# Kernel tuning notes

Measured on AMD Instinct MI355X. Metric: run time of the kernel, lower is better.

Reference implementation:

```python
import jax, jax.numpy as jnp
import numpy as np

N_NODES = 50000
N_EDGES = 800000
IN_FEATURES = 256
HIDDEN = 128


def setup_inputs() -> dict:
    key = jax.random.key(0)
    k_x, k_r, k_c, k_v, k_w, k_b = jax.random.split(key, 6)
    x = jax.random.normal(k_x, (N_NODES, IN_FEATURES), dtype=jnp.float32)
    adj_row = jax.random.randint(k_r, (N_EDGES,), 0, N_NODES, dtype=jnp.int32)
    adj_col = jax.random.randint(k_c, (N_EDGES,), 0, N_NODES, dtype=jnp.int32)
    adj_val = jax.random.uniform(k_v, (N_EDGES,), dtype=jnp.float32)
    # Linear params: weight [hidden, in_features] (xavier-normal-ish), bias [hidden]
    std = float(np.sqrt(2.0 / (IN_FEATURES + HIDDEN)))
    W = jax.random.normal(k_w, (HIDDEN, IN_FEATURES), dtype=jnp.float32) * std
    b = jax.random.normal(k_b, (HIDDEN,), dtype=jnp.float32) * 0.01
    return {"x": x, "adj_row": adj_row, "adj_col": adj_col, "adj_val": adj_val, "W": W, "b": b}


def reference(x, adj_row, adj_col, adj_val, W, b):
    # support = Linear(x): [N, hidden]
    support = jnp.einsum('nf,hf->nh', x, W) + b
    # sparse adj @ support via edge-list gather + segment-sum scatter
    gathered = support[adj_col] * adj_val[:, None]          # [E, hidden]
    out = jax.ops.segment_sum(gathered, adj_row, num_segments=N_NODES)  # [N, hidden]
    return out
```

## Files before the change

kernel.cpp:

```cpp
#include <hip/hip_runtime.h>

#define N_NODES 50000
#define N_EDGES 800000
#define IN_F    256
#define HIDDEN  128

#define BUCKET_SZ 64
#define NB        782
#define NBINS     1024
#define EBLOCK    3328
#define EPT       13
#define EBLOCKS   241
#define LIN_ROWS  128
#define LBLOCKS   391
#define NTASKS    632
#define OFST_W    256
#define CAP       1300

#define SMEM_BYTES 35840

typedef __attribute__((ext_vector_type(8))) short bf16x8;
typedef __attribute__((ext_vector_type(4))) float f32x4;

__device__ inline unsigned short f2bf(float f) {
    unsigned u = __float_as_uint(f);
    u += 0x7FFF + ((u >> 16) & 1);
    return (unsigned short)(u >> 16);
}
__device__ inline bf16x8 cvt8(float4 a, float4 b) {
    bf16x8 r;
    r[0] = (short)f2bf(a.x); r[1] = (short)f2bf(a.y);
    r[2] = (short)f2bf(a.z); r[3] = (short)f2bf(a.w);
    r[4] = (short)f2bf(b.x); r[5] = (short)f2bf(b.y);
    r[6] = (short)f2bf(b.z); r[7] = (short)f2bf(b.w);
    return r;
}
__device__ inline float bfLo(unsigned u) { return __uint_as_float(u << 16); }
__device__ inline float bfHi(unsigned u) { return __uint_as_float(u & 0xFFFF0000u); }

__global__ __launch_bounds__(256) void fused_linear_partition_kernel(
    const float* __restrict__ x, const float* __restrict__ W,
    const float* __restrict__ bias, unsigned short* __restrict__ support,
    const int* __restrict__ adj_row, const int* __restrict__ adj_col,
    const float* __restrict__ adj_val,
    int2* __restrict__ part, int* __restrict__ ofsT)
{
    __shared__ __align__(16) char smem[SMEM_BYTES];
    const int tid = threadIdx.x;

    if (blockIdx.x < EBLOCKS) {
        int2* lbuf = (int2*)smem;
        int*  lofs = (int*)(smem + 26624);
        int*  lcur = (int*)(smem + 30720);
        int*  tsum = (int*)(smem + 34816);

        const int task = blockIdx.x;
        const int base = task * EBLOCK;
        const int n    = min(EBLOCK, N_EDGES - base);

        for (int i = tid; i < NBINS; i += 256) lofs[i] = 0;
        __syncthreads();

        unsigned pk[EPT]; float pv[EPT];
#pragma unroll
        for (int i = 0; i < EPT; ++i) {
            int li = tid + i * 256;
            bool ok = li < n;
            int ee = ok ? (base + li) : base;
            int r = adj_row[ee], c = adj_col[ee];
            float v = adj_val[ee];
            if (ok) {
                unsigned bk = (unsigned)r >> 6;
                pk[i] = (bk << 22) | (((unsigned)r & 63u) << 16) | (unsigned)c;
                pv[i] = v;
                atomicAdd(&lofs[bk], 1);
            } else pk[i] = 0xFFFFFFFFu;
        }
        __syncthreads();

        int s0 = lofs[tid * 4], s1 = lofs[tid * 4 + 1];
        int s2 = lofs[tid * 4 + 2], s3 = lofs[tid * 4 + 3];
        int mysum = s0 + s1 + s2 + s3;
        tsum[tid] = mysum;
        __syncthreads();
#pragma unroll
        for (int off = 1; off < 256; off <<= 1) {
            int t = (tid >= off) ? tsum[tid - off] : 0;
            __syncthreads();
            tsum[tid] += t;
            __syncthreads();
        }
        int ex = tsum[tid] - mysum;
        lofs[tid * 4]     = ex;
        lofs[tid * 4 + 1] = ex + s0;
        lofs[tid * 4 + 2] = ex + s0 + s1;
        lofs[tid * 4 + 3] = ex + s0 + s1 + s2;
        __syncthreads();

        for (int i = tid; i < NBINS; i += 256) lcur[i] = lofs[i];
        __syncthreads();

#pragma unroll
        for (int i = 0; i < EPT; ++i) {
            if (pk[i] != 0xFFFFFFFFu) {
                unsigned bk = pk[i] >> 22;
                int p = atomicAdd(&lcur[bk], 1);
                lbuf[p] = make_int2((int)(pk[i] & 0x3FFFFF), __float_as_int(pv[i]));
            }
        }
        __syncthreads();

        for (int j = tid; j < n; j += 256)
            part[(size_t)task * EBLOCK + j] = lbuf[j];
        for (int i = tid; i <= NB; i += 256)
            ofsT[(size_t)i * OFST_W + task] = lofs[i];
    } else {
        short* wfrag = (short*)smem;

        const int bid  = blockIdx.x - EBLOCKS;
        const int lane = tid & 63;
        const int wave = tid >> 6;
        const int quad = lane >> 4;
        const int l16  = lane & 15;

        int m0 = bid * LIN_ROWS + wave * 32 + l16;
        int m1 = m0 + 16;
        if (m0 >= N_NODES) m0 = N_NODES - 1;
        if (m1 >= N_NODES) m1 = N_NODES - 1;
        const float* xr0 = x + (size_t)m0 * IN_F;
        const float* xr1 = x + (size_t)m1 * IN_F;

        f32x4 acc[2][8];
#pragma unroll
        for (int g = 0; g < 2; ++g)
#pragma unroll
            for (int s = 0; s < 8; ++s) acc[g][s] = (f32x4){0.f, 0.f, 0.f, 0.f};

#pragma unroll
        for (int half = 0; half < 2; ++half) {
#pragma unroll
            for (int it = 0; it < 8; ++it) {
                const int f   = it * 256 + tid;
                const int ln  = f & 63;
                const int s   = (f >> 6) & 7;
                const int kc  = f >> 9;
                const int row = s * 16 + (ln & 15);
                const int k0  = (half * 4 + kc) * 32 + (ln >> 4) * 8;
                const float* wp = W + (size_t)row * IN_F + k0;
                float4 b0 = *(const float4*)wp;
                float4 b1 = *(const float4*)(wp + 4);
                *(bf16x8*)(&wfrag[(size_t)f * 8]) = cvt8(b0, b1);
            }
            __syncthreads();

#pragma unroll
            for (int kc = 0; kc < 4; ++kc) {
                const int k0 = (half * 4 + kc) * 32 + quad * 8;
                float4 a0 = *(const float4*)(xr0 + k0);
                float4 a1 = *(const float4*)(xr0 + k0 + 4);
                bf16x8 af0 = cvt8(a0, a1);
                float4 a2 = *(const float4*)(xr1 + k0);
                float4 a3 = *(const float4*)(xr1 + k0 + 4);
                bf16x8 af1 = cvt8(a2, a3);
                const short* bbase = &wfrag[((size_t)(kc * 8) * 64 + lane) * 8];
#pragma unroll
                for (int s = 0; s < 8; ++s) {
                    bf16x8 bf = *(const bf16x8*)(bbase + (size_t)s * 64 * 8);
                    acc[0][s] = __builtin_amdgcn_mfma_f32_16x16x32_bf16(af0, bf, acc[0][s], 0, 0, 0);
                    acc[1][s] = __builtin_amdgcn_mfma_f32_16x16x32_bf16(af1, bf, acc[1][s], 0, 0, 0);
                }
            }
            __syncthreads();
        }

#pragma unroll
        for (int g = 0; g < 2; ++g) {
            const int rowBase = bid * LIN_ROWS + wave * 32 + g * 16 + quad * 4;
#pragma unroll
            for (int reg = 0; reg < 4; ++reg) {
                const int r = rowBase + reg;
                if (r < N_NODES) {
#pragma unroll
                    for (int s = 0; s < 8; ++s) {
                        const int col = s * 16 + l16;
                        float v = acc[g][s][reg] + bias[col];
                        support[(size_t)r * HIDDEN + col] = f2bf(v);
                    }
                }
            }
        }
    }
}

__global__ __launch_bounds__(512) void bucket_gather_kernel(
    const int* __restrict__ ofsT, const int2* __restrict__ part,
    const unsigned int* __restrict__ support_u32, float* __restrict__ out)
{
    __shared__ int2 sbufA[CAP];
    __shared__ int2 sbufB[CAP];
    __shared__ int  wsum[8];
    __shared__ int  hist[BUCKET_SZ];
    __shared__ int  rp[BUCKET_SZ + 1];
    __shared__ int  cur[BUCKET_SZ];

    const int tid  = threadIdx.x;
    const int b    = blockIdx.x;
    const int wave = tid >> 6;
    const int lane = tid & 63;

    if (tid < BUCKET_SZ) hist[tid] = 0;

    int s0 = 0, slen = 0;
    if (tid < EBLOCKS) {
        s0   = ofsT[(size_t)b * OFST_W + tid];
        slen = ofsT[(size_t)(b + 1) * OFST_W + tid] - s0;
    }

    int iv = slen;
#pragma unroll
    for (int off = 1; off < 64; off <<= 1) {
        int t = __shfl_up(iv, off);
        if (lane >= off) iv += t;
    }
    if (lane == 63) wsum[wave] = iv;
    __syncthreads();
    int wpre = 0, total = 0;
#pragma unroll
    for (int w = 0; w < 8; ++w) {
        int sw = wsum[w];
        total += sw;
        if (w < wave) wpre += sw;
    }
    const int excl = wpre + iv - slen;
    const int n    = min(total, CAP);

    {
        const int2* seg = part + (size_t)tid * EBLOCK + s0;
        for (int k = 0; k < slen; ++k) {
            int p = excl + k;
            if (p < CAP) {
                int2 cv = seg[k];
                sbufA[p] = cv;
                atomicAdd(&hist[(cv.x >> 16) & 63], 1);
            }
        }
    }
    __syncthreads();

    if (tid < 64) {
        int a = hist[tid];
        int ia = a;
#pragma unroll
        for (int off = 1; off < 64; off <<= 1) {
            int t = __shfl_up(ia, off);
            if (tid >= off) ia += t;
        }
        rp[tid + 1] = ia;
        if (tid == 0) rp[0] = 0;
        cur[tid] = ia - a;
    }
    __syncthreads();

    for (int j = tid; j < n; j += 512) {
        int2 cv = sbufA[j];
        int p = atomicAdd(&cur[(cv.x >> 16) & 63], 1);
        sbufB[p] = cv;
    }
    __syncthreads();

    const int rowLo = wave * 8;
#pragma unroll 1
    for (int r = rowLo; r < rowLo + 8; ++r) {
        const int grow = b * BUCKET_SZ + r;
        if (grow >= N_NODES) break;
        const int s = rp[r], e = rp[r + 1];
        float ax = 0.f, ay = 0.f;
        int j = s;
        for (; j + 7 < e; j += 8) {
            int2 c0 = sbufB[j],     c1 = sbufB[j + 1];
            int2 c2 = sbufB[j + 2], c3 = sbufB[j + 3];
            int2 c4 = sbufB[j + 4], c5 = sbufB[j + 5];
            int2 c6 = sbufB[j + 6], c7 = sbufB[j + 7];
            unsigned u0 = support_u32[(size_t)(c0.x & 0xFFFF) * 64 + lane];
            unsigned u1 = support_u32[(size_t)(c1.x & 0xFFFF) * 64 + lane];
            unsigned u2 = support_u32[(size_t)(c2.x & 0xFFFF) * 64 + lane];
            unsigned u3 = support_u32[(size_t)(c3.x & 0xFFFF) * 64 + lane];
            unsigned u4 = support_u32[(size_t)(c4.x & 0xFFFF) * 64 + lane];
            unsigned u5 = support_u32[(size_t)(c5.x & 0xFFFF) * 64 + lane];
            unsigned u6 = support_u32[(size_t)(c6.x & 0xFFFF) * 64 + lane];
            unsigned u7 = support_u32[(size_t)(c7.x & 0xFFFF) * 64 + lane];
            float v0 = __int_as_float(c0.y), v1 = __int_as_float(c1.y);
            float v2 = __int_as_float(c2.y), v3 = __int_as_float(c3.y);
            float v4 = __int_as_float(c4.y), v5 = __int_as_float(c5.y);
            float v6 = __int_as_float(c6.y), v7 = __int_as_float(c7.y);
            ax += v0 * bfLo(u0); ay += v0 * bfHi(u0);
            ax += v1 * bfLo(u1); ay += v1 * bfHi(u1);
            ax += v2 * bfLo(u2); ay += v2 * bfHi(u2);
            ax += v3 * bfLo(u3); ay += v3 * bfHi(u3);
            ax += v4 * bfLo(u4); ay += v4 * bfHi(u4);
            ax += v5 * bfLo(u5); ay += v5 * bfHi(u5);
            ax += v6 * bfLo(u6); ay += v6 * bfHi(u6);
            ax += v7 * bfLo(u7); ay += v7 * bfHi(u7);
        }
        for (; j + 3 < e; j += 4) {
            int2 c0 = sbufB[j],     c1 = sbufB[j + 1];
            int2 c2 = sbufB[j + 2], c3 = sbufB[j + 3];
            unsigned u0 = support_u32[(size_t)(c0.x & 0xFFFF) * 64 + lane];
            unsigned u1 = support_u32[(size_t)(c1.x & 0xFFFF) * 64 + lane];
            unsigned u2 = support_u32[(size_t)(c2.x & 0xFFFF) * 64 + lane];
            unsigned u3 = support_u32[(size_t)(c3.x & 0xFFFF) * 64 + lane];
            float v0 = __int_as_float(c0.y), v1 = __int_as_float(c1.y);
            float v2 = __int_as_float(c2.y), v3 = __int_as_float(c3.y);
            ax += v0 * bfLo(u0); ay += v0 * bfHi(u0);
            ax += v1 * bfLo(u1); ay += v1 * bfHi(u1);
            ax += v2 * bfLo(u2); ay += v2 * bfHi(u2);
            ax += v3 * bfLo(u3); ay += v3 * bfHi(u3);
        }
        for (; j < e; ++j) {
            int2 cv = sbufB[j];
            unsigned u = support_u32[(size_t)(cv.x & 0xFFFF) * 64 + lane];
            float v = __int_as_float(cv.y);
            ax += v * bfLo(u); ay += v * bfHi(u);
        }
        *(float2*)(out + (size_t)grow * HIDDEN + lane * 2) = make_float2(ax, ay);
    }
}

extern "C" void kernel_launch(void* const* d_in, const int* in_sizes, int n_in,
                              void* d_out, int out_size, void* d_ws, size_t ws_size,
                              hipStream_t stream) {
    const float* x       = (const float*)d_in[0];
    const int*   adj_row = (const int*)d_in[1];
    const int*   adj_col = (const int*)d_in[2];
    const float* adj_val = (const float*)d_in[3];
    const float* W       = (const float*)d_in[4];
    const float* b       = (const float*)d_in[5];
    float* out = (float*)d_out;

    char* wsb = (char*)d_ws;
    const size_t off_support = 0;
    const size_t off_part    = off_support + (size_t)N_NODES * HIDDEN * 2;
    const size_t off_ofsT    = off_part + (size_t)EBLOCKS * EBLOCK * 8;

    unsigned short* support = (unsigned short*)(wsb + off_support);
    int2* part = (int2*)(wsb + off_part);
    int*  ofsT = (int*)(wsb + off_ofsT);

    fused_linear_partition_kernel<<<NTASKS, 256, 0, stream>>>(
        x, W, b, support, adj_row, adj_col, adj_val, part, ofsT);
    bucket_gather_kernel<<<NB, 512, 0, stream>>>(
        ofsT, part, (const unsigned int*)support, out);
}
```

Measured before the change: 159.0 us.

## Pre-convert W to bf16 fragments in separate kernel, read from global in linear blocks

Adds a small kernel that converts W to bf16 MFMA fragment layout once per call. The linear blocks now load B fragments directly from global/L2 instead of each block converting W into LDS with barriers. The rows per block are halved to 64, doubling the number of linear blocks, and occupancy is hinted to 4 blocks/CU. The trade-off is an extra kernel launch and repeated global reads of the fragments, which rely on L2/cache hits.

```diff
diff --git a/kernel.cpp b/kernel.cpp
--- a/kernel.cpp
+++ b/kernel.cpp
@@ -11,11 +11,12 @@
 #define EBLOCK    3328
 #define EPT       13
 #define EBLOCKS   241
-#define LIN_ROWS  128
-#define LBLOCKS   391
-#define NTASKS    632
+#define LIN_ROWS  64
+#define LBLOCKS   782
+#define NTASKS    1023
 #define OFST_W    256
 #define CAP       1300
+#define NFRAG     4096
 
 #define SMEM_BYTES 35840
 
@@ -38,17 +39,33 @@
 __device__ inline float bfLo(unsigned u) { return __uint_as_float(u << 16); }
 __device__ inline float bfHi(unsigned u) { return __uint_as_float(u & 0xFFFF0000u); }
 
-__global__ __launch_bounds__(256) void fused_linear_partition_kernel(
-    const float* __restrict__ x, const float* __restrict__ W,
+__global__ __launch_bounds__(256) void wconv_kernel(
+    const float* __restrict__ W, unsigned short* __restrict__ wb)
+{
+    const int f = blockIdx.x * 256 + threadIdx.x;
+    if (f >= NFRAG) return;
+    const int ln = f & 63;
+    const int s  = (f >> 6) & 7;
+    const int hk = f >> 9;
+    const int row = s * 16 + (ln & 15);
+    const int k0  = hk * 32 + (ln >> 4) * 8;
+    const float* wp = W + (size_t)row * IN_F + k0;
+    float4 b0 = *(const float4*)wp;
+    float4 b1 = *(const float4*)(wp + 4);
+    *(bf16x8*)(wb + (size_t)f * 8) = cvt8(b0, b1);
+}
+
+__global__ __launch_bounds__(256, 4) void fused_linear_partition_kernel(
+    const float* __restrict__ x, const unsigned short* __restrict__ wb,
     const float* __restrict__ bias, unsigned short* __restrict__ support,
     const int* __restrict__ adj_row, const int* __restrict__ adj_col,
     const float* __restrict__ adj_val,
     int2* __restrict__ part, int* __restrict__ ofsT)
 {
-    __shared__ __align__(16) char smem[SMEM_BYTES];
     const int tid = threadIdx.x;
 
     if (blockIdx.x < EBLOCKS) {
+        __shared__ __align__(16) char smem[SMEM_BYTES];
         int2* lbuf = (int2*)smem;
         int*  lofs = (int*)(smem + 26624);
         int*  lcur = (int*)(smem + 30720);
@@ -115,77 +132,45 @@
         for (int i = tid; i <= NB; i += 256)
             ofsT[(size_t)i * OFST_W + task] = lofs[i];
     } else {
-        short* wfrag = (short*)smem;
-
         const int bid  = blockIdx.x - EBLOCKS;
         const int lane = tid & 63;
         const int wave = tid >> 6;
         const int quad = lane >> 4;
         const int l16  = lane & 15;
 
-        int m0 = bid * LIN_ROWS + wave * 32 + l16;
-        int m1 = m0 + 16;
-        if (m0 >= N_NODES) m0 = N_NODES - 1;
-        if (m1 >= N_NODES) m1 = N_NODES - 1;
-        const float* xr0 = x + (size_t)m0 * IN_F;
-        const float* xr1 = x + (size_t)m1 * IN_F;
-
-        f32x4 acc[2][8];
-#pragma unroll
-        for (int g = 0; g < 2; ++g)
-#pragma unroll
-            for (int s = 0; s < 8; ++s) acc[g][s] = (f32x4){0.f, 0.f, 0.f, 0.f};
-
-#pragma unroll
-        for (int half = 0; half < 2; ++half) {
-#pragma unroll
-            for (int it = 0; it < 8; ++it) {
-                const int f   = it * 256 + tid;
-                const int ln  = f & 63;
-                const int s   = (f >> 6) & 7;
-                const int kc  = f >> 9;
-                const int row = s * 16 + (ln & 15);
-                const int k0  = (half * 4 + kc) * 32 + (ln >> 4) * 8;
-                const float* wp = W + (size_t)row * IN_F + k0;
-                float4 b0 = *(const float4*)wp;
-                float4 b1 = *(const float4*)(wp + 4);
-                *(bf16x8*)(&wfrag[(size_t)f * 8]) = cvt8(b0, b1);
+        int m = bid * LIN_ROWS + wave * 16 + l16;
+        if (m >= N_NODES) m = N_NODES - 1;
+        const float* xrow = x + (size_t)m * IN_F;
+        const bf16x8* wbv = (const bf16x8*)wb;
+
+        f32x4 acc[8];
+#pragma unroll
+        for (int s = 0; s < 8; ++s) acc[s] = (f32x4){0.f, 0.f, 0.f, 0.f};
+
+#pragma unroll 2
+        for (int hk = 0; hk < 8; ++hk) {
+            const int k0 = hk * 32 + quad * 8;
+            float4 a0 = *(const float4*)(xrow + k0);
+            float4 a1 = *(const float4*)(xrow + k0 + 4);
+            bf16x8 af = cvt8(a0, a1);
+            const bf16x8* bb = wbv + (size_t)hk * 512 + lane;
+#pragma unroll
+            for (int s = 0; s < 8; ++s) {
+                bf16x8 bf = bb[(size_t)s * 64];
+                acc[s] = __builtin_amdgcn_mfma_f32_16x16x32_bf16(af, bf, acc[s], 0, 0, 0);
             }
-            __syncthreads();
-
-#pragma unroll
-            for (int kc = 0; kc < 4; ++kc) {
-                const int k0 = (half * 4 + kc) * 32 + quad * 8;
-                float4 a0 = *(const float4*)(xr0 + k0);
-                float4 a1 = *(const float4*)(xr0 + k0 + 4);
-                bf16x8 af0 = cvt8(a0, a1);
-                float4 a2 = *(const float4*)(xr1 + k0);
-                float4 a3 = *(const float4*)(xr1 + k0 + 4);
-                bf16x8 af1 = cvt8(a2, a3);
-                const short* bbase = &wfrag[((size_t)(kc * 8) * 64 + lane) * 8];
+        }
+
+        const int rowBase = bid * LIN_ROWS + wave * 16 + quad * 4;
+#pragma unroll
+        for (int reg = 0; reg < 4; ++reg) {
+            const int r = rowBase + reg;
+            if (r < N_NODES) {
 #pragma unroll
                 for (int s = 0; s < 8; ++s) {
-                    bf16x8 bf = *(const bf16x8*)(bbase + (size_t)s * 64 * 8);
-                    acc[0][s] = __builtin_amdgcn_mfma_f32_16x16x32_bf16(af0, bf, acc[0][s], 0, 0, 0);
-                    acc[1][s] = __builtin_amdgcn_mfma_f32_16x16x32_bf16(af1, bf, acc[1][s], 0, 0, 0);
-                }
-            }
-            __syncthreads();
-        }
-
-#pragma unroll
-        for (int g = 0; g < 2; ++g) {
-            const int rowBase = bid * LIN_ROWS + wave * 32 + g * 16 + quad * 4;
-#pragma unroll
-            for (int reg = 0; reg < 4; ++reg) {
-                const int r = rowBase + reg;
-                if (r < N_NODES) {
-#pragma unroll
-                    for (int s = 0; s < 8; ++s) {
-                        const int col = s * 16 + l16;
-                        float v = acc[g][s][reg] + bias[col];
-                        support[(size_t)r * HIDDEN + col] = f2bf(v);
-                    }
+                    const int col = s * 16 + l16;
+                    float v = acc[s][reg] + bias[col];
+                    support[(size_t)r * HIDDEN + col] = f2bf(v);
                 }
             }
         }
@@ -341,13 +326,16 @@
     const size_t off_support = 0;
     const size_t off_part    = off_support + (size_t)N_NODES * HIDDEN * 2;
     const size_t off_ofsT    = off_part + (size_t)EBLOCKS * EBLOCK * 8;
+    const size_t off_wb      = off_ofsT + (size_t)(NB + 1) * OFST_W * 4;
 
     unsigned short* support = (unsigned short*)(wsb + off_support);
     int2* part = (int2*)(wsb + off_part);
     int*  ofsT = (int*)(wsb + off_ofsT);
-
+    unsigned short* wb = (unsigned short*)(wsb + off_wb);
+
+    wconv_kernel<<<NFRAG / 256, 256, 0, stream>>>(W, wb);
     fused_linear_partition_kernel<<<NTASKS, 256, 0, stream>>>(
-        x, W, b, support, adj_row, adj_col, adj_val, part, ofsT);
+        x, wb, b, support, adj_row, adj_col, adj_val, part, ofsT);
     bucket_gather_kernel<<<NB, 512, 0, stream>>>(
         ofsT, part, (const unsigned int*)support, out);
 }
```

Measured after the change: 156.1 us. About the same (-1.8%).
